# Kernel optimization log

Measured on AMD Instinct MI355X. Metric: run time of the kernel, lower is better.

The kernel has to match this reference:

```python
import jax, jax.numpy as jnp
import numpy as np
import math

EMBED_DIM = 2048
NUM_HEADS = 16
HEAD_DIM = EMBED_DIM // NUM_HEADS
BATCH = 2
SEQ = 2048


def setup_inputs() -> dict:
    key = jax.random.key(0)
    ks = jax.random.split(key, 6)
    x = jax.random.normal(ks[0], (BATCH, SEQ, EMBED_DIM), dtype=jnp.float32)
    # causal mask: True = masked (upper triangle, strictly above diagonal)
    attn_mask = jnp.triu(jnp.ones((SEQ, SEQ), dtype=bool), k=1)
    s = 1.0 / math.sqrt(EMBED_DIM)
    W_qkv = jax.random.normal(ks[1], (3 * EMBED_DIM, EMBED_DIM), dtype=jnp.float32) * s
    b_qkv = jax.random.normal(ks[2], (3 * EMBED_DIM,), dtype=jnp.float32) * 0.01
    W_out = jax.random.normal(ks[3], (EMBED_DIM, EMBED_DIM), dtype=jnp.float32) * s
    b_out = jax.random.normal(ks[4], (EMBED_DIM,), dtype=jnp.float32) * 0.01
    return {"x": x, "W_qkv": W_qkv, "b_qkv": b_qkv, "W_out": W_out,
            "b_out": b_out, "attn_mask": attn_mask}


def reference(x, W_qkv, b_qkv, W_out, b_out, attn_mask):
    B, S, E = x.shape
    # fused QKV projection: [B,S,3E]
    qkv = jnp.einsum('bse,fe->bsf', x, W_qkv) + b_qkv
    qkv = qkv.reshape(B, S, 3, NUM_HEADS, HEAD_DIM)
    qkv = jnp.transpose(qkv, (2, 0, 3, 1, 4))  # [3,B,H,S,Dh]
    q, k, v = qkv[0], qkv[1], qkv[2]
    scale = 1.0 / math.sqrt(HEAD_DIM)
    scores = jnp.einsum('bhqd,bhkd->bhqk', q, k) * scale  # [B,H,S,S]
    scores = jnp.where(attn_mask[None, None, :, :], -jnp.inf, scores)
    attn = jax.nn.softmax(scores, axis=-1)
    out = jnp.einsum('bhqk,bhkd->bhqd', attn, v)  # [B,H,S,Dh]
    out = jnp.transpose(out, (0, 2, 1, 3)).reshape(B, S, E)
    out = jnp.einsum('bse,fe->bsf', out, W_out) + b_out
    return out
```

## Files before the change

### kernel.cpp

```cpp
#include <hip/hip_runtime.h>
#include <hip/hip_bf16.h>
#include <math.h>

#define SEQ   2048
#define EMBED 2048
#define NHEAD 16
#define DHEAD 128
#define BATCH 2

#define NX   ((size_t)BATCH * SEQ * EMBED)
#define NW1  ((size_t)3 * EMBED * EMBED)
#define NB1  ((size_t)3 * EMBED)
#define NW2  ((size_t)EMBED * EMBED)
#define NB2  ((size_t)EMBED)

typedef __bf16 bf16;
typedef __attribute__((__ext_vector_type__(8))) __bf16 bf16x8;
typedef __attribute__((__ext_vector_type__(4))) __bf16 bf16x4;
typedef __attribute__((__ext_vector_type__(4))) float f32x4;
typedef __attribute__((__ext_vector_type__(4))) unsigned int u32x4;

#define NEG_BIG (-1.0e30f)

__device__ __forceinline__ f32x4 mfma_16x16x32(bf16x8 a, bf16x8 b, f32x4 c) {
  return __builtin_amdgcn_mfma_f32_16x16x32_bf16(a, b, c, 0, 0, 0);
}

__device__ __forceinline__ void llds16(bf16* dst, const bf16* src) {
  __builtin_amdgcn_global_load_lds(
      (const __attribute__((address_space(1))) void*)src,
      (__attribute__((address_space(3))) void*)dst, 16, 0, 0);
}

#define BARRAW() asm volatile("s_barrier" ::: "memory")

__global__ void convert_inputs(const void* __restrict__ xin,
                               const void* __restrict__ w1in,
                               const void* __restrict__ b1in,
                               const void* __restrict__ w2in,
                               const void* __restrict__ b2in,
                               bf16* __restrict__ xb, bf16* __restrict__ w1b,
                               bf16* __restrict__ b1b, bf16* __restrict__ w2b,
                               bf16* __restrict__ b2b, int* __restrict__ flagp)
{
  __shared__ int sflag;
  if (threadIdx.x == 0) sflag = 0;
  __syncthreads();
  const unsigned short* xh = (const unsigned short*)xin;
  int huge = 0;
  for (int i = threadIdx.x; i < 2048; i += 256) {
    float f = __uint_as_float((unsigned int)xh[i] << 16);
    if (!(fabsf(f) <= 1e4f)) huge = 1;
  }
  if (huge) sflag = 1;
  __syncthreads();
  const int isf32 = sflag;
  if (blockIdx.x == 0 && threadIdx.x == 0) *flagp = isf32;

  const void* srcs[5] = {xin, w1in, b1in, w2in, b2in};
  bf16* dsts[5] = {xb, w1b, b1b, w2b, b2b};
  const size_t lens[5] = {NX, NW1, NB1, NW2, NB2};
  const size_t gid = (size_t)blockIdx.x * blockDim.x + threadIdx.x;
  const size_t gstride = (size_t)gridDim.x * blockDim.x;
  for (int sidx = 0; sidx < 5; ++sidx) {
    const size_t n8 = lens[sidx] >> 3;
    bf16* d = dsts[sidx];
    if (isf32) {
      const float* s = (const float*)srcs[sidx];
      for (size_t i = gid; i < n8; i += gstride) {
        const float* sp = s + i * 8;
        bf16x8 r;
#pragma unroll
        for (int j = 0; j < 8; ++j) r[j] = (bf16)sp[j];
        *(bf16x8*)(d + i * 8) = r;
      }
    } else {
      const u32x4* s = (const u32x4*)srcs[sidx];
      for (size_t i = gid; i < n8; i += gstride)
        *(u32x4*)(d + i * 8) = s[i];
    }
  }
}

__global__ __launch_bounds__(512, 1) void gemmM(
    const bf16* __restrict__ A, const bf16* __restrict__ B,
    const bf16* __restrict__ bias,
    bf16* __restrict__ outq, bf16* __restrict__ outk, bf16* __restrict__ outv)
{
  __shared__ __align__(16) bf16 lds_[65536];
  const int t = threadIdx.x;
  const int lane = t & 63, w = t >> 6;
  const int wm = w >> 2, wn = w & 3;
  const int lr = lane & 15, lq = lane >> 4;
  const int f = blockIdx.x;
  const int o = (f & 7) * 48 + (f >> 3);
  const int by = o & 15, bx = o >> 4;
  const int m0 = by << 8, n0 = bx << 8;
  const int K = EMBED;
  const int NT = K >> 6;

  const int sg8 = ((lane & 3) ^ (((lane >> 5) & 1) << 1)) << 3;
  const bf16* aS  = A + (size_t)(m0 + w * 32 + (lane >> 2)) * K + sg8;
  const bf16* aS2 = aS + (size_t)16 * K;
  const bf16* bS  = B + (size_t)(n0 + w * 32 + (lane >> 2)) * K + sg8;
  const bf16* bS2 = bS + (size_t)16 * K;
  const int dA = w * 1024;
  const int dB = 16384 + w * 1024;

#define STAGE_HALF(kt_, ks_)                                                 \
  {                                                                          \
    const int _bufb = ((kt_) & 1) * 32768 + (ks_) * 8192;                    \
    const int _kc = ((kt_) << 6) + (ks_) * 32;                               \
    llds16(lds_ + _bufb + dA, aS + _kc);                                     \
    llds16(lds_ + _bufb + dA + 512, aS2 + _kc);                              \
    llds16(lds_ + _bufb + dB, bS + _kc);                                     \
    llds16(lds_ + _bufb + dB + 512, bS2 + _kc);                              \
  }

  f32x4 acc[8][4];
#pragma unroll
  for (int i = 0; i < 8; ++i)
#pragma unroll
    for (int j = 0; j < 4; ++j) acc[i][j] = (f32x4){0.f, 0.f, 0.f, 0.f};

  const int rg8 = (lq ^ (((lr >> 3) & 1) << 1)) << 3;
  const int arow_ = (wm * 128 + lr) * 32 + rg8;
  const int brow_ = 16384 + (wn * 64 + lr) * 32 + rg8;

  STAGE_HALF(0, 0);
  STAGE_HALF(0, 1);
  asm volatile("s_waitcnt vmcnt(0)" ::: "memory");
  BARRAW();

  for (int tt = 0; tt < NT; ++tt) {
    const int bufb = (tt & 1) * 32768;
#pragma unroll
    for (int ks = 0; ks < 2; ++ks) {
      const int base = bufb + ks * 8192;
      bf16x8 af[8], bfv[4];
#pragma unroll
      for (int ai = 0; ai < 8; ++ai)
        af[ai] = *(const bf16x8*)(lds_ + base + arow_ + ai * 512);
#pragma unroll
      for (int ni = 0; ni < 4; ++ni)
        bfv[ni] = *(const bf16x8*)(lds_ + base + brow_ + ni * 512);
      if (tt + 1 < NT) STAGE_HALF(tt + 1, ks);
      __builtin_amdgcn_s_setprio(1);
#pragma unroll
      for (int ai = 0; ai < 8; ++ai)
#pragma unroll
        for (int ni = 0; ni < 4; ++ni)
          acc[ai][ni] = mfma_16x16x32(af[ai], bfv[ni], acc[ai][ni]);
      __builtin_amdgcn_s_setprio(0);
      if (tt + 1 < NT) {
        asm volatile("s_waitcnt vmcnt(4)" ::: "memory");
      } else if (ks == 0) {
        asm volatile("s_waitcnt vmcnt(0)" ::: "memory");
      }
      BARRAW();
    }
  }
#undef STAGE_HALF

  const int which = n0 >> 11;
  const int bbid = m0 >> 11;
  const int s0 = m0 & 2047;
  if (which == 2) {
#pragma unroll
    for (int ni = 0; ni < 4; ++ni) {
      const int ng = n0 + wn * 64 + ni * 16 + lr;
      const int h = (ng >> 7) & 15;
      const int d = ng & 127;
      const float bv = (float)bias[ng];
      bf16* rowp =
          outv + ((size_t)(bbid * NHEAD + h) * DHEAD + d) * SEQ + s0 + wm * 128;
#pragma unroll
      for (int ai = 0; ai < 8; ++ai) {
        bf16x4 pk;
#pragma unroll
        for (int reg = 0; reg < 4; ++reg)
          pk[reg] = (bf16)(acc[ai][ni][reg] + bv);
        *(bf16x4*)(rowp + ai * 16 + lq * 4) = pk;
      }
    }
  } else {
    bf16* dst = (which == 0) ? outq : outk;
#pragma unroll
    for (int ni = 0; ni < 4; ++ni) {
      const int ng = n0 + wn * 64 + ni * 16 + lr;
      const int h = (ng >> 7) & 15;
      const int d = ng & 127;
      const float bv = (float)bias[ng];
      bf16* hb = dst + (size_t)(bbid * NHEAD + h) * SEQ * DHEAD + d;
#pragma unroll
      for (int ai = 0; ai < 8; ++ai)
#pragma unroll
        for (int reg = 0; reg < 4; ++reg) {
          const int s = s0 + wm * 128 + ai * 16 + lq * 4 + reg;
          hb[(size_t)s * DHEAD] = (bf16)(acc[ai][ni][reg] + bv);
        }
    }
  }
}

template <int MODE>
__global__ __launch_bounds__(512, 1) void gemmE(
    const bf16* __restrict__ A, const bf16* __restrict__ B,
    const bf16* __restrict__ bias, int K,
    void* __restrict__ out0v, bf16* __restrict__ out1, bf16* __restrict__ out2,
    const int* __restrict__ flagp)
{
  __shared__ __align__(16) bf16 lds_[49152];
  constexpr int NTX = (MODE == 0) ? 24 : 8;
  const int t = threadIdx.x;
  const int lane = t & 63, w = t >> 6;
  const int wm = w >> 2, wn = w & 3;
  const int lr = lane & 15, lq = lane >> 4;
  const int nwg = 32 * NTX;
  const int f = blockIdx.x;
  const int o = (f & 7) * (nwg >> 3) + (f >> 3);
  const int by = o & 31, bx = o >> 5;
  const int m0 = by << 7, n0 = bx << 8;
  const int NT = K >> 6;
  const int NI = NT >> 1;

  const int srow = t >> 2;
  const int sg8 = (((t & 3) ^ (((t >> 5) & 1) << 1))) << 3;

#define STAGE3(kt_, ks_)                                                     \
  {                                                                          \
    const int _kt = (kt_), _ks = (ks_);                                      \
    if (_kt < NT) {                                                          \
      const int _bb = (_kt & 1) * 24576;                                     \
      const int _kc = (_kt << 6) + _ks * 32;                                 \
      llds16(lds_ + _bb + _ks * 4096 + (w << 9),                             \
             A + (size_t)(m0 + srow) * K + _kc + sg8);                       \
      llds16(lds_ + _bb + 8192 + _ks * 8192 + (w << 9),                      \
             B + (size_t)(n0 + srow) * K + _kc + sg8);                       \
      llds16(lds_ + _bb + 8192 + _ks * 8192 + 4096 + (w << 9),               \
             B + (size_t)(n0 + 128 + srow) * K + _kc + sg8);                 \
    }                                                                        \
  }

  f32x4 acc[4][4];
#pragma unroll
  for (int i = 0; i < 4; ++i)
#pragma unroll
    for (int j = 0; j < 4; ++j) acc[i][j] = (f32x4){0.f, 0.f, 0.f, 0.f};

  const int rg8 = ((lq ^ (((lr >> 3) & 1) << 1))) << 3;
  const int arow = (wm * 64 + lr) * 32 + rg8;
  const int brow = (wn * 64 + lr) * 32 + rg8;

  STAGE3(0, 0);
  STAGE3(0, 1);
  STAGE3(1, 0);
  asm volatile("s_waitcnt vmcnt(6)" ::: "memory");
  BARRAW();

  for (int i = 0; i < NI; ++i) {
    const int k2 = i << 1;
#pragma unroll
    for (int p = 0; p < 4; ++p) {
      const int ks = p & 1;
      const int bufb = (p >> 1) * 24576;
      bf16x8 af[4], bfv[4];
      const int ab = bufb + ks * 4096 + arow;
      const int bb = bufb + 8192 + ks * 8192 + brow;
#pragma unroll
      for (int mi = 0; mi < 4; ++mi)
        af[mi] = *(const bf16x8*)(lds_ + ab + mi * 512);
#pragma unroll
      for (int ni = 0; ni < 4; ++ni)
        bfv[ni] = *(const bf16x8*)(lds_ + bb + ni * 512);
      if (p == 0)      STAGE3(k2 + 1, 1)
      else if (p == 1) STAGE3(k2 + 2, 0)
      else if (p == 2) STAGE3(k2 + 2, 1)
      else             STAGE3(k2 + 3, 0)
      BARRAW();
      __builtin_amdgcn_s_setprio(1);
#pragma unroll
      for (int mi = 0; mi < 4; ++mi)
#pragma unroll
        for (int ni = 0; ni < 4; ++ni)
          acc[mi][ni] = mfma_16x16x32(af[mi], bfv[ni], acc[mi][ni]);
      __builtin_amdgcn_s_setprio(0);
      if (i == 0 && p == 0) {
        asm volatile("s_waitcnt vmcnt(6)" ::: "memory");
      }
      if (p == 1) {
        if (i == NI - 1) { asm volatile("s_waitcnt vmcnt(0)" ::: "memory"); }
        else             { asm volatile("s_waitcnt vmcnt(3)" ::: "memory"); }
      }
      if (p == 3 && i < NI - 1) {
        asm volatile("s_waitcnt vmcnt(3)" ::: "memory");
      }
      BARRAW();
    }
  }
#undef STAGE3

  if (MODE == 0) {
    const int which = n0 >> 11;
    const int bbid = m0 >> 11;
    const int s0 = m0 & 2047;
    if (which == 2) {
      bf16* dst = out2;
#pragma unroll
      for (int ni = 0; ni < 4; ++ni) {
        const int ng = n0 + wn * 64 + ni * 16 + lr;
        const int h = (ng >> 7) & 15;
        const int d = ng & 127;
        const float bv = (float)bias[ng];
        bf16* rowp =
            dst + ((size_t)(bbid * NHEAD + h) * DHEAD + d) * SEQ + s0 + wm * 64;
#pragma unroll
        for (int mi = 0; mi < 4; ++mi) {
          bf16x4 pk;
#pragma unroll
          for (int reg = 0; reg < 4; ++reg)
            pk[reg] = (bf16)(acc[mi][ni][reg] + bv);
          *(bf16x4*)(rowp + mi * 16 + lq * 4) = pk;
        }
      }
    } else {
      bf16* dst = (which == 0) ? (bf16*)out0v : out1;
#pragma unroll
      for (int ni = 0; ni < 4; ++ni) {
        const int ng = n0 + wn * 64 + ni * 16 + lr;
        const int h = (ng >> 7) & 15;
        const int d = ng & 127;
        const float bv = (float)bias[ng];
        bf16* hb = dst + (size_t)(bbid * NHEAD + h) * SEQ * DHEAD + d;
#pragma unroll
        for (int mi = 0; mi < 4; ++mi)
#pragma unroll
          for (int reg = 0; reg < 4; ++reg) {
            const int s = s0 + wm * 64 + mi * 16 + lq * 4 + reg;
            hb[(size_t)s * DHEAD] = (bf16)(acc[mi][ni][reg] + bv);
          }
      }
    }
  } else {
    const int isf32 = *flagp;
#pragma unroll
    for (int ni = 0; ni < 4; ++ni) {
      const int col = n0 + wn * 64 + ni * 16 + lr;
      const float bv = (float)bias[col];
#pragma unroll
      for (int mi = 0; mi < 4; ++mi)
#pragma unroll
        for (int reg = 0; reg < 4; ++reg) {
          const int row = m0 + wm * 64 + mi * 16 + lq * 4 + reg;
          const float v = acc[mi][ni][reg] + bv;
          const size_t idx = (size_t)row * EMBED + col;
          if (isf32) ((float*)out0v)[idx] = v;
          else       ((bf16*)out0v)[idx] = (bf16)v;
        }
    }
  }
}

__device__ __forceinline__ void qk_softmax_tile(
    const bf16* __restrict__ sK, bf16* __restrict__ sP, const bf16x8* aq,
    float& m_i, float& l_i, f32x4* oacc, int kt, int qt,
    int w, int lr, int lq, int sPofs)
{
  const float scale = 0.08838834764831845f;
  f32x4 tacc[4];
#pragma unroll
  for (int ni = 0; ni < 4; ++ni) tacc[ni] = (f32x4){0.f, 0.f, 0.f, 0.f};
#pragma unroll
  for (int ks = 0; ks < 4; ++ks)
#pragma unroll
    for (int ni = 0; ni < 4; ++ni) {
      bf16x8 bk = *(const bf16x8*)(sK + (ni * 16 + lr) * 136 + ks * 32 + lq * 8);
      tacc[ni] = mfma_16x16x32(bk, aq[ks], tacc[ni]);
    }
  float pp[4][4];
  const int qg = qt * 64 + w * 16 + lr;
#pragma unroll
  for (int ni = 0; ni < 4; ++ni)
#pragma unroll
    for (int reg = 0; reg < 4; ++reg) {
      float sv = tacc[ni][reg] * scale;
      if (kt == qt) {
        const int kg = kt * 64 + ni * 16 + lq * 4 + reg;
        if (kg > qg) sv = NEG_BIG;
      }
      pp[ni][reg] = sv;
    }
  float mx;
  {
    float a0 = fmaxf(fmaxf(pp[0][0], pp[0][1]), fmaxf(pp[0][2], pp[0][3]));
    float a1 = fmaxf(fmaxf(pp[1][0], pp[1][1]), fmaxf(pp[1][2], pp[1][3]));
    float a2 = fmaxf(fmaxf(pp[2][0], pp[2][1]), fmaxf(pp[2][2], pp[2][3]));
    float a3 = fmaxf(fmaxf(pp[3][0], pp[3][1]), fmaxf(pp[3][2], pp[3][3]));
    mx = fmaxf(fmaxf(a0, a1), fmaxf(a2, a3));
  }
  mx = fmaxf(mx, __shfl_xor(mx, 16, 64));
  mx = fmaxf(mx, __shfl_xor(mx, 32, 64));
  const float mnew = fmaxf(m_i, mx);
  const float alpha = __expf(m_i - mnew);
  float ls = 0.f;
#pragma unroll
  for (int ni = 0; ni < 4; ++ni) {
    float s0 = __expf(pp[ni][0] - mnew);
    float s1 = __expf(pp[ni][1] - mnew);
    float s2 = __expf(pp[ni][2] - mnew);
    float s3 = __expf(pp[ni][3] - mnew);
    pp[ni][0] = s0; pp[ni][1] = s1; pp[ni][2] = s2; pp[ni][3] = s3;
    ls += (s0 + s1) + (s2 + s3);
  }
  ls += __shfl_xor(ls, 16, 64);
  ls += __shfl_xor(ls, 32, 64);
  l_i = l_i * alpha + ls;
  m_i = mnew;
#pragma unroll
  for (int dt = 0; dt < 8; ++dt) oacc[dt] *= alpha;
  bf16* rowp = sP + (sPofs + w * 16 + lr) * 64;
  const int swz = lr & 7;
#pragma unroll
  for (int ni = 0; ni < 4; ++ni) {
    bf16x4 pk;
#pragma unroll
    for (int reg = 0; reg < 4; ++reg) pk[reg] = (bf16)pp[ni][reg];
    const int col = ni * 16 + lq * 4;
    const int scol = (((col >> 3) ^ swz) << 3) | (col & 7);
    *(bf16x4*)(rowp + scol) = pk;
  }
}

__device__ __forceinline__ void pv_tile(const bf16* __restrict__ sP,
                                        const bf16* __restrict__ sV,
                                        f32x4* oacc, int w, int lr, int lq,
                                        int sPofs)
{
  const bf16* rowp = sP + (sPofs + w * 16 + lr) * 64;
  const int swz = lr & 7;
#pragma unroll
  for (int ks2 = 0; ks2 < 2; ++ks2) {
    const int chunk = ks2 * 4 + lq;
    bf16x8 bp = *(const bf16x8*)(rowp + ((chunk ^ swz) << 3));
#pragma unroll
    for (int dt = 0; dt < 8; ++dt) {
      bf16x8 av =
          *(const bf16x8*)(sV + (dt * 16 + lr) * 72 + ks2 * 32 + lq * 8);
      oacc[dt] = mfma_16x16x32(av, bp, oacc[dt]);
    }
  }
}

__global__ __launch_bounds__(256, 2) void attn_fwd(
    const bf16* __restrict__ qb, const bf16* __restrict__ kb,
    const bf16* __restrict__ vt, bf16* __restrict__ aout)
{
  __shared__ bf16 sK[64 * 136];
  __shared__ bf16 sV[128 * 72];
  __shared__ bf16 sP[128 * 64];
  const int t = threadIdx.x;
  const int lane = t & 63, w = t >> 6;
  const int lr = lane & 15, lq = lane >> 4;
  const int p  = blockIdx.x & 15;
  const int bh = blockIdx.x >> 4;
  const int bb = bh >> 4, h = bh & 15;
  const int qlo = p, qhi = 31 - p;

  bf16x8 aqL[4], aqH[4];
  {
    const bf16* qpL =
        qb + ((size_t)bh * SEQ + qlo * 64 + w * 16 + lr) * DHEAD + lq * 8;
    const bf16* qpH =
        qb + ((size_t)bh * SEQ + qhi * 64 + w * 16 + lr) * DHEAD + lq * 8;
#pragma unroll
    for (int ks = 0; ks < 4; ++ks) {
      aqL[ks] = *(const bf16x8*)(qpL + ks * 32);
      aqH[ks] = *(const bf16x8*)(qpH + ks * 32);
    }
  }

  f32x4 oL[8], oH[8];
#pragma unroll
  for (int i = 0; i < 8; ++i) {
    oL[i] = (f32x4){0.f, 0.f, 0.f, 0.f};
    oH[i] = (f32x4){0.f, 0.f, 0.f, 0.f};
  }
  float mL = NEG_BIG, mH = NEG_BIG;
  float lL = 0.f, lH = 0.f;

  bf16x8 rk[4], rv[4];
  const int kr_ = t >> 4, kd_ = t & 15;
  const int vr_ = t >> 3, vk_ = t & 7;
#define FETCH(ktv)                                                          \
  {                                                                         \
    const int _kt = (ktv);                                                  \
    _Pragma("unroll") for (int i = 0; i < 4; ++i) {                         \
      rk[i] = *(const bf16x8*)(kb + ((size_t)bh * SEQ + _kt * 64 +          \
                                     (i * 16 + kr_)) * DHEAD + kd_ * 8);    \
      rv[i] = *(const bf16x8*)(vt + ((size_t)bh * DHEAD + (i * 32 + vr_)) * \
                                     SEQ + _kt * 64 + vk_ * 8);             \
    }                                                                       \
  }
#define COMMIT()                                                            \
  {                                                                         \
    _Pragma("unroll") for (int i = 0; i < 4; ++i) {                         \
      *(bf16x8*)(sK + (i * 16 + kr_) * 136 + kd_ * 8) = rk[i];              \
      *(bf16x8*)(sV + (i * 32 + vr_) * 72 + vk_ * 8) = rv[i];               \
    }                                                                       \
  }

  FETCH(0);
  COMMIT();
  __syncthreads();

  for (int kt = 0; kt <= qhi; ++kt) {
    if (kt < qhi) FETCH(kt + 1);
    const bool doLo = (kt <= qlo);

    qk_softmax_tile(sK, sP, aqH, mH, lH, oH, kt, qhi, w, lr, lq, 64);
    if (doLo) qk_softmax_tile(sK, sP, aqL, mL, lL, oL, kt, qlo, w, lr, lq, 0);
    asm volatile("s_waitcnt lgkmcnt(0)" ::: "memory");
    pv_tile(sP, sV, oH, w, lr, lq, 64);
    if (doLo) pv_tile(sP, sV, oL, w, lr, lq, 0);

    __syncthreads();
    if (kt < qhi) {
      COMMIT();
      __syncthreads();
    }
  }

#pragma unroll
  for (int side = 0; side < 2; ++side) {
    const f32x4* oacc = side ? oH : oL;
    const float linv = 1.0f / (side ? lH : lL);
    const int qt = side ? qhi : qlo;
    const int qg = qt * 64 + w * 16 + lr;
    bf16* outp = aout + ((size_t)bb * SEQ + qg) * EMBED + h * 128 + lq * 4;
#pragma unroll
    for (int dt = 0; dt < 8; ++dt) {
      bf16x4 pk;
#pragma unroll
      for (int reg = 0; reg < 4; ++reg)
        pk[reg] = (bf16)(oacc[dt][reg] * linv);
      *(bf16x4*)(outp + dt * 16) = pk;
    }
  }
#undef FETCH
#undef COMMIT
}

extern "C" void kernel_launch(void* const* d_in, const int* in_sizes, int n_in,
                              void* d_out, int out_size, void* d_ws, size_t ws_size,
                              hipStream_t stream) {
  const void* x    = d_in[0];
  const void* Wqkv = d_in[1];
  const void* bqkv = d_in[2];
  const void* Wout = d_in[3];
  const void* bout = d_in[4];

  int* flagp = (int*)d_ws;
  bf16* base = (bf16*)((char*)d_ws + 256);
  bf16* xb   = base;
  bf16* w1b  = xb + NX;
  bf16* b1b  = w1b + NW1;
  bf16* w2b  = b1b + NB1;
  bf16* b2b  = w2b + NW2;
  bf16* qb   = b2b + NB2;
  bf16* kb   = qb + NX;
  bf16* vt   = kb + NX;
  bf16* aout = vt + NX;

  convert_inputs<<<dim3(1024), dim3(256), 0, stream>>>(
      x, Wqkv, bqkv, Wout, bout, xb, w1b, b1b, w2b, b2b, flagp);
  gemmM<<<dim3(384), dim3(512), 0, stream>>>(xb, w1b, b1b, qb, kb, vt);
  attn_fwd<<<dim3(512), dim3(256), 0, stream>>>(qb, kb, vt, aout);
  gemmE<1><<<dim3(256), dim3(512), 0, stream>>>(
      aout, w2b, b2b, EMBED, d_out, nullptr, nullptr, flagp);
}
```

Measured before the change: 388.7 us.

## Software-pipeline GEMM LDS fragments, lazy softmax rescale, MFMA priority, block remap

The GEMM main loop is restructured to keep even and odd k-slice A fragments in separate register sets. The next slice's LDS reads are issued before the current MFMAs, with finer waitcnts and one extra stage prefetched, so LDS latency hides behind MFMA work. In attention, the online-softmax rescale is skipped unless the running max grows by more than a threshold (the FA4-style lazy rescale), and s_setprio is raised around the QK and PV MFMA blocks. Attention blocks are also remapped across the grid (likely to spread them across XCDs). This raises register pressure and the lazy rescale relies on exp not overflowing within the threshold.

```diff
diff --git a/kernel.cpp b/kernel.cpp
--- a/kernel.cpp
+++ b/kernel.cpp
@@ -127,38 +127,59 @@
   const int arow_ = (wm * 128 + lr) * 32 + rg8;
   const int brow_ = 16384 + (wn * 64 + lr) * 32 + rg8;
 
+  bf16x8 afE[8], afO[8], bfv[4];
+
   STAGE_HALF(0, 0);
   STAGE_HALF(0, 1);
-  asm volatile("s_waitcnt vmcnt(0)" ::: "memory");
+  STAGE_HALF(1, 0);
+  asm volatile("s_waitcnt vmcnt(4)" ::: "memory");
   BARRAW();
-
+#pragma unroll
+  for (int ai = 0; ai < 8; ++ai)
+    afE[ai] = *(const bf16x8*)(lds_ + arow_ + ai * 512);
+
+#pragma unroll 1
   for (int tt = 0; tt < NT; ++tt) {
     const int bufb = (tt & 1) * 32768;
-#pragma unroll
-    for (int ks = 0; ks < 2; ++ks) {
-      const int base = bufb + ks * 8192;
-      bf16x8 af[8], bfv[4];
+    const int nbufb = bufb ^ 32768;
+#pragma unroll
+    for (int ni = 0; ni < 4; ++ni)
+      bfv[ni] = *(const bf16x8*)(lds_ + bufb + brow_ + ni * 512);
+#pragma unroll
+    for (int ai = 0; ai < 8; ++ai)
+      afO[ai] = *(const bf16x8*)(lds_ + bufb + 8192 + arow_ + ai * 512);
+    if (tt + 1 < NT) STAGE_HALF(tt + 1, 1);
+    asm volatile("s_waitcnt lgkmcnt(8)" ::: "memory");
+    __builtin_amdgcn_sched_barrier(0);
+    __builtin_amdgcn_s_setprio(1);
+#pragma unroll
+    for (int ai = 0; ai < 8; ++ai)
+#pragma unroll
+      for (int ni = 0; ni < 4; ++ni)
+        acc[ai][ni] = mfma_16x16x32(afE[ai], bfv[ni], acc[ai][ni]);
+    __builtin_amdgcn_s_setprio(0);
+    asm volatile("s_waitcnt vmcnt(4)" ::: "memory");
+    BARRAW();
+#pragma unroll
+    for (int ni = 0; ni < 4; ++ni)
+      bfv[ni] = *(const bf16x8*)(lds_ + bufb + 8192 + brow_ + ni * 512);
+    if (tt + 1 < NT) {
 #pragma unroll
       for (int ai = 0; ai < 8; ++ai)
-        af[ai] = *(const bf16x8*)(lds_ + base + arow_ + ai * 512);
+        afE[ai] = *(const bf16x8*)(lds_ + nbufb + arow_ + ai * 512);
+    }
+    if (tt + 2 < NT) STAGE_HALF(tt + 2, 0);
+    asm volatile("s_waitcnt lgkmcnt(8)" ::: "memory");
+    __builtin_amdgcn_sched_barrier(0);
+    __builtin_amdgcn_s_setprio(1);
+#pragma unroll
+    for (int ai = 0; ai < 8; ++ai)
 #pragma unroll
       for (int ni = 0; ni < 4; ++ni)
-        bfv[ni] = *(const bf16x8*)(lds_ + base + brow_ + ni * 512);
-      if (tt + 1 < NT) STAGE_HALF(tt + 1, ks);
-      __builtin_amdgcn_s_setprio(1);
-#pragma unroll
-      for (int ai = 0; ai < 8; ++ai)
-#pragma unroll
-        for (int ni = 0; ni < 4; ++ni)
-          acc[ai][ni] = mfma_16x16x32(af[ai], bfv[ni], acc[ai][ni]);
-      __builtin_amdgcn_s_setprio(0);
-      if (tt + 1 < NT) {
-        asm volatile("s_waitcnt vmcnt(4)" ::: "memory");
-      } else if (ks == 0) {
-        asm volatile("s_waitcnt vmcnt(0)" ::: "memory");
-      }
-      BARRAW();
-    }
+        acc[ai][ni] = mfma_16x16x32(afO[ai], bfv[ni], acc[ai][ni]);
+    __builtin_amdgcn_s_setprio(0);
+    asm volatile("s_waitcnt vmcnt(4)" ::: "memory");
+    BARRAW();
   }
 #undef STAGE_HALF
 
@@ -370,6 +391,7 @@
   f32x4 tacc[4];
 #pragma unroll
   for (int ni = 0; ni < 4; ++ni) tacc[ni] = (f32x4){0.f, 0.f, 0.f, 0.f};
+  __builtin_amdgcn_s_setprio(1);
 #pragma unroll
   for (int ks = 0; ks < 4; ++ks)
 #pragma unroll
@@ -377,6 +399,7 @@
       bf16x8 bk = *(const bf16x8*)(sK + (ni * 16 + lr) * 136 + ks * 32 + lq * 8);
       tacc[ni] = mfma_16x16x32(bk, aq[ks], tacc[ni]);
     }
+  __builtin_amdgcn_s_setprio(0);
   float pp[4][4];
   const int qg = qt * 64 + w * 16 + lr;
 #pragma unroll
@@ -400,24 +423,27 @@
   }
   mx = fmaxf(mx, __shfl_xor(mx, 16, 64));
   mx = fmaxf(mx, __shfl_xor(mx, 32, 64));
-  const float mnew = fmaxf(m_i, mx);
-  const float alpha = __expf(m_i - mnew);
+  if (!__all(mx <= m_i + 8.0f)) {
+    const float mnew = fmaxf(m_i, mx);
+    const float alpha = __expf(m_i - mnew);
+    l_i *= alpha;
+#pragma unroll
+    for (int dt = 0; dt < 8; ++dt) oacc[dt] *= alpha;
+    m_i = mnew;
+  }
   float ls = 0.f;
 #pragma unroll
   for (int ni = 0; ni < 4; ++ni) {
-    float s0 = __expf(pp[ni][0] - mnew);
-    float s1 = __expf(pp[ni][1] - mnew);
-    float s2 = __expf(pp[ni][2] - mnew);
-    float s3 = __expf(pp[ni][3] - mnew);
+    float s0 = __expf(pp[ni][0] - m_i);
+    float s1 = __expf(pp[ni][1] - m_i);
+    float s2 = __expf(pp[ni][2] - m_i);
+    float s3 = __expf(pp[ni][3] - m_i);
     pp[ni][0] = s0; pp[ni][1] = s1; pp[ni][2] = s2; pp[ni][3] = s3;
     ls += (s0 + s1) + (s2 + s3);
   }
   ls += __shfl_xor(ls, 16, 64);
   ls += __shfl_xor(ls, 32, 64);
-  l_i = l_i * alpha + ls;
-  m_i = mnew;
-#pragma unroll
-  for (int dt = 0; dt < 8; ++dt) oacc[dt] *= alpha;
+  l_i += ls;
   bf16* rowp = sP + (sPofs + w * 16 + lr) * 64;
   const int swz = lr & 7;
 #pragma unroll
@@ -438,6 +464,7 @@
 {
   const bf16* rowp = sP + (sPofs + w * 16 + lr) * 64;
   const int swz = lr & 7;
+  __builtin_amdgcn_s_setprio(1);
 #pragma unroll
   for (int ks2 = 0; ks2 < 2; ++ks2) {
     const int chunk = ks2 * 4 + lq;
@@ -449,6 +476,7 @@
       oacc[dt] = mfma_16x16x32(av, bp, oacc[dt]);
     }
   }
+  __builtin_amdgcn_s_setprio(0);
 }
 
 __global__ __launch_bounds__(256, 2) void attn_fwd(
@@ -461,8 +489,10 @@
   const int t = threadIdx.x;
   const int lane = t & 63, w = t >> 6;
   const int lr = lane & 15, lq = lane >> 4;
-  const int p  = blockIdx.x & 15;
-  const int bh = blockIdx.x >> 4;
+  const int f = blockIdx.x;
+  const int o = (f & 7) * 64 + (f >> 3);
+  const int p  = o & 15;
+  const int bh = o >> 4;
   const int bb = bh >> 4, h = bh & 15;
   const int qlo = p, qhi = 31 - p;
 
```

Measured after the change: 400.2 us. 3.0% more time.
